# Kernel optimization log

Hardware: AMD Instinct MI355X
Metric: run time of the kernel (lower is better)

Reference implementation:

```python
import jax, jax.numpy as jnp
import numpy as np

BETA = 1.0
EPS = 1e-12  # F.normalize eps

def _normalize(x):
    # F.normalize(x, dim=1): x shape (B, N, 1)
    n = jnp.sqrt(jnp.sum(x * x, axis=1, keepdims=True))
    return x / jnp.maximum(n, EPS)

def _step(M, x):
    return _normalize(jnp.matmul(M, x))

def _eigval(M, x):
    # x^T M x / ||x||^2, x: (B, N, 1)
    Mx = jnp.matmul(M, x)                          # (B, N, 1)
    num = jnp.sum(Mx * x, axis=(1, 2))             # (B,)
    den = jnp.sum(x * x, axis=(1, 2))              # (B,)
    return num / den

def setup_inputs() -> dict:
    key = jax.random.key(0)
    kA, kx = jax.random.split(key)
    A = jax.random.normal(kA, (64, 512, 28, 28), dtype=jnp.float32)
    x0 = jax.random.normal(kx, (64, 512, 1), dtype=jnp.float32)
    return {"A": A, "x0": x0}

def reference(A, x0):
    B, C, H, W = A.shape
    Wm = A.reshape(B, C, H * W)                    # (B, C, HW)
    AAT = jnp.einsum('bcd,bed->bce', Wm, Wm)       # (B, C, C)

    # --- dominant_eigenvalue(AAT): first call initializes last_x (no grad, 3 iters) ---
    xi = _normalize(x0)
    for _ in range(3):
        xi = _step(AAT, xi)
    xi = jax.lax.stop_gradient(xi)                 # last_x after no-grad init
    x1 = _step(AAT, xi)                            # 1 differentiable iter
    largest = _eigval(AAT, x1)                     # (B,)
    last_x = jax.lax.stop_gradient(x1)             # self.last_x = x.detach()

    # --- dominant_eigenvalue(AAT - largest*I): reuses last_x, 1 iter ---
    I = jnp.eye(C, dtype=A.dtype)[None]            # (1, C, C)
    A2 = AAT - largest[:, None, None] * I
    x2 = _step(A2, last_x)
    tmp = _eigval(A2, x2)

    smallest = tmp + largest
    penalty = BETA * (largest / smallest - 1.0) ** 2
    return jnp.sum(penalty) / B
```

## Files before the change

### kernel.cpp

```cpp
#include <hip/hip_runtime.h>
#include <math.h>


#define BB 64
#define CC 512
#define DD 784
#define DCH 16
#define NCH 49
#define NSPLIT 8
#define F4PR 196
#define FEPS 1e-12f

__device__ __forceinline__ void gload16(const float4* gp, float4* lp) {
    __builtin_amdgcn_global_load_lds(
        (const __attribute__((address_space(1))) void*)gp,
        (__attribute__((address_space(3))) void*)lp, 16, 0, 0);
}

__device__ __forceinline__ float blk_reduce(float s, float* red) {
    for (int off = 32; off; off >>= 1) s += __shfl_down(s, off, 64);
    int w = threadIdx.x >> 6;
    if ((threadIdx.x & 63) == 0) red[w] = s;
    __syncthreads();
    float t = red[0] + red[1] + red[2] + red[3];
    __syncthreads();
    return t;
}

__global__ __launch_bounds__(256, 2)
void k_step(const float* __restrict__ A, const float* __restrict__ xin,
            const int nparts, float* __restrict__ vout) {
    __shared__ float xs[CC];
    __shared__ float tile[2][CC * DCH];
    __shared__ float uw[4][DCH];
    __shared__ float usd[DCH];
    __shared__ float red[4];

    const int tid = threadIdx.x;
    const int b = blockIdx.y;
    const int s = blockIdx.x;
    const int lane = tid & 63;
    const int w = tid >> 6;
    const int rr = tid >> 2, widx = tid & 3;

    const float4* Ap = (const float4*)(A + (size_t)b * CC * DD);

    {
        float4* lbase = &((float4*)tile[0])[w * 64];
        const float4* gbase = Ap + (size_t)rr * F4PR + s * 4 + widx;
#pragma unroll
        for (int i = 0; i < 8; i++)
            gload16(gbase + (size_t)i * 64 * F4PR, lbase + i * 256);
    }

    const float* xp = xin + (size_t)b * nparts * CC;
    float xv0 = 0.f, xv1 = 0.f;
    for (int p = 0; p < nparts; p++) {
        xv0 += xp[p * CC + tid];
        xv1 += xp[p * CC + tid + 256];
    }
    float ss = blk_reduce(xv0 * xv0 + xv1 * xv1, red);
    float rn = 1.0f / fmaxf(sqrtf(ss), FEPS);
    xs[tid] = xv0 * rn;
    xs[tid + 256] = xv1 * rn;

    float v0 = 0.f, v1 = 0.f;
    int buf = 0;
    const int c0 = tid, c1 = tid + 256;
    const int lh = lane >> 1;

    for (int ch = s; ch < NCH; ch += NSPLIT) {
        const int nxt = ch + NSPLIT;
        if (nxt < NCH) {
            float4* lbase = &((float4*)tile[buf ^ 1])[w * 64];
            const float4* gbase = Ap + (size_t)rr * F4PR + nxt * 4 + widx;
#pragma unroll
            for (int i = 0; i < 8; i++)
                gload16(gbase + (size_t)i * 64 * F4PR, lbase + i * 256);
            __builtin_amdgcn_sched_barrier(0);
            asm volatile("s_waitcnt vmcnt(8)" ::: "memory");
        } else {
            __builtin_amdgcn_sched_barrier(0);
            asm volatile("s_waitcnt vmcnt(0)" ::: "memory");
        }
        asm volatile("s_waitcnt lgkmcnt(0)" ::: "memory");
        __builtin_amdgcn_s_barrier();
        __builtin_amdgcn_sched_barrier(0);

        float4 ua = make_float4(0.f, 0.f, 0.f, 0.f);
        const float4* t4p = (const float4*)tile[buf];
#pragma unroll
        for (int i = 0; i < 8; i++) {
            float4 a4 = t4p[tid + i * 256];
            float x = xs[rr + i * 64];
            ua.x += a4.x * x; ua.y += a4.y * x;
            ua.z += a4.z * x; ua.w += a4.w * x;
        }
#pragma unroll
        for (int off = 4; off <= 32; off <<= 1) {
            ua.x += __shfl_xor(ua.x, off, 64);
            ua.y += __shfl_xor(ua.y, off, 64);
            ua.z += __shfl_xor(ua.z, off, 64);
            ua.w += __shfl_xor(ua.w, off, 64);
        }
        if (lane < 4) {
            uw[w][lane * 4 + 0] = ua.x; uw[w][lane * 4 + 1] = ua.y;
            uw[w][lane * 4 + 2] = ua.z; uw[w][lane * 4 + 3] = ua.w;
        }
        __builtin_amdgcn_sched_barrier(0);
        asm volatile("s_waitcnt lgkmcnt(0)" ::: "memory");
        __builtin_amdgcn_s_barrier();
        __builtin_amdgcn_sched_barrier(0);

        if (tid < DCH)
            usd[tid] = uw[0][tid] + uw[1][tid] + uw[2][tid] + uw[3][tid];
        __builtin_amdgcn_sched_barrier(0);
        asm volatile("s_waitcnt lgkmcnt(0)" ::: "memory");
        __builtin_amdgcn_s_barrier();
        __builtin_amdgcn_sched_barrier(0);

        const float* tp = tile[buf];
#pragma unroll
        for (int k = 0; k < DCH; k++) {
            int d = (k + lh) & (DCH - 1);
            float ud = usd[d];
            v0 += tp[c0 * DCH + d] * ud;
            v1 += tp[c1 * DCH + d] * ud;
        }
        __builtin_amdgcn_sched_barrier(0);
        asm volatile("s_waitcnt lgkmcnt(0)" ::: "memory");
        __builtin_amdgcn_s_barrier();
        __builtin_amdgcn_sched_barrier(0);
        buf ^= 1;
    }

    float* vp = vout + ((size_t)b * NSPLIT + s) * CC;
    vp[c0] = v0;
    vp[c1] = v1;
}

__global__ void k_mid(const float* __restrict__ t4, const float* __restrict__ t5,
                      float* __restrict__ acc, float* __restrict__ y) {
    __shared__ float red[4];
    int b = blockIdx.x;
    const float* p4 = t4 + (size_t)b * NSPLIT * CC;
    const float* p5 = t5 + (size_t)b * NSPLIT * CC;
    float a0 = 0.f, a1 = 0.f, b0 = 0.f, b1 = 0.f;
    for (int p = 0; p < NSPLIT; p++) {
        a0 += p4[p * CC + threadIdx.x]; a1 += p4[p * CC + threadIdx.x + 256];
        b0 += p5[p * CC + threadIdx.x]; b1 += p5[p * CC + threadIdx.x + 256];
    }
    float ss4 = blk_reduce(a0 * a0 + a1 * a1, red);
    float rn = 1.0f / fmaxf(sqrtf(ss4), FEPS);
    float x10 = a0 * rn, x11 = a1 * rn;
    float num = blk_reduce(b0 * x10 + b1 * x11, red);
    float den = blk_reduce(x10 * x10 + x11 * x11, red);
    float largest = num / den;
    float* yp = y + (size_t)b * CC;
    yp[threadIdx.x] = b0 - largest * x10;
    yp[threadIdx.x + 256] = b1 - largest * x11;
    if (threadIdx.x == 0) acc[b * 8 + 0] = largest;
}

__global__ void k_fin2(const float* __restrict__ w, const float* __restrict__ y,
                       float* __restrict__ acc) {
    __shared__ float red[4];
    int b = blockIdx.x;
    const float* wp = w + (size_t)b * NSPLIT * CC;
    const float* yp = y + (size_t)b * CC;
    float w0 = 0.f, w1 = 0.f;
    for (int p = 0; p < NSPLIT; p++) {
        w0 += wp[p * CC + threadIdx.x];
        w1 += wp[p * CC + threadIdx.x + 256];
    }
    float y0 = yp[threadIdx.x], y1 = yp[threadIdx.x + 256];
    float ssy = blk_reduce(y0 * y0 + y1 * y1, red);
    float rn = 1.0f / fmaxf(sqrtf(ssy), FEPS);
    float x20 = y0 * rn, x21 = y1 * rn;
    float dotwx = blk_reduce(w0 * x20 + w1 * x21, red);
    float den2 = blk_reduce(x20 * x20 + x21 * x21, red);
    if (threadIdx.x == 0) { acc[b * 8 + 1] = dotwx; acc[b * 8 + 2] = den2; }
}

__global__ void k_out(const float* __restrict__ acc, float* __restrict__ out) {
    int b = threadIdx.x;
    float largest = acc[b * 8 + 0];
    float dotwx   = acc[b * 8 + 1];
    float den2    = acc[b * 8 + 2];
    float tmp = (dotwx - largest * den2) / den2;
    float smallest = tmp + largest;
    float r = largest / smallest - 1.0f;
    float pen = r * r;
    for (int off = 32; off; off >>= 1) pen += __shfl_down(pen, off, 64);
    if (b == 0) out[0] = pen / (float)BB;
}

extern "C" void kernel_launch(void* const* d_in, const int* in_sizes, int n_in,
                              void* d_out, int out_size, void* d_ws, size_t ws_size,
                              hipStream_t stream) {
    const float* A  = (const float*)d_in[0];
    const float* x0 = (const float*)d_in[1];
    float* out = (float*)d_out;
    float* ws = (float*)d_ws;

    float* acc = ws;
    float* y   = ws + 512;
    float* PA  = y + BB * CC;
    float* PB  = PA + BB * NSPLIT * CC;

    dim3 gS(NSPLIT, BB);
    k_step<<<gS, 256, 0, stream>>>(A, x0, 1, PA);
    k_step<<<gS, 256, 0, stream>>>(A, PA, NSPLIT, PB);
    k_step<<<gS, 256, 0, stream>>>(A, PB, NSPLIT, PA);
    k_step<<<gS, 256, 0, stream>>>(A, PA, NSPLIT, PB);
    k_step<<<gS, 256, 0, stream>>>(A, PB, NSPLIT, PA);

    k_mid<<<BB, 256, 0, stream>>>(PB, PA, acc, y);

    k_step<<<gS, 256, 0, stream>>>(A, y, 1, PB);

    k_fin2<<<BB, 256, 0, stream>>>(PB, y, acc);
    k_out<<<1, 64, 0, stream>>>(acc, out);
}
```

Measured before the change: 324.8 us.

## Repack A into chunk-contiguous layout and vectorize second GEMV LDS reads

Adds a repack kernel that rewrites A per batch into contiguous 512x16 column chunks, so each step kernel streams fully contiguous memory instead of strided row segments. The step kernels switch to 7 splits of 7 contiguous chunks each and read the tile as float4 in the second reduction, with a per-wave copy of the u vector that removes one block barrier. The cost is an extra full pass over A (read and write of about 100MB) per call and a large workspace, with a fallback to the old layout when the workspace is too small.

```diff
diff --git a/kernel.cpp b/kernel.cpp
--- a/kernel.cpp
+++ b/kernel.cpp
@@ -6,9 +6,11 @@
 #define CC 512
 #define DD 784
 #define DCH 16
-#define NCH 49
-#define NSPLIT 8
+#define NSPLIT 7
+#define NCHPS 7
 #define F4PR 196
+#define CHF4 2048
+#define BF4 100352
 #define FEPS 1e-12f
 
 __device__ __forceinline__ void gload16(const float4* gp, float4* lp) {
@@ -27,31 +29,64 @@
     return t;
 }
 
+__global__ __launch_bounds__(256, 3)
+void k_repack(const float* __restrict__ A, float* __restrict__ T) {
+    __shared__ float4 st4[4 * 784];
+    const int tid = threadIdx.x, lane = tid & 63, w = tid >> 6;
+    const int b = blockIdx.y, slab = blockIdx.x;
+    const int R = slab * 16 + w * 4;
+    const float4* src = (const float4*)A + ((size_t)b * CC + R) * F4PR;
+    float4* stw = st4 + w * 784;
+#pragma unroll
+    for (int i = 0; i < 12; i++)
+        gload16(src + i * 64 + lane, stw + i * 64);
+    if (lane < 16) gload16(src + 768 + lane, stw + 768);
+    __builtin_amdgcn_sched_barrier(0);
+    asm volatile("s_waitcnt vmcnt(0)" ::: "memory");
+    __builtin_amdgcn_sched_barrier(0);
+    float4* dst = (float4*)T + (size_t)b * BF4;
+#pragma unroll
+    for (int i = 0; i < 13; i++) {
+        int m = i * 64 + lane;
+        if (m < 784) {
+            int ch = m >> 4, rem = m & 15, r = rem >> 2, dq = rem & 3;
+            dst[(size_t)ch * CHF4 + (size_t)(R + r) * 4 + dq] =
+                stw[r * 196 + ch * 4 + dq];
+        }
+    }
+}
+
+template <bool RP>
 __global__ __launch_bounds__(256, 2)
-void k_step(const float* __restrict__ A, const float* __restrict__ xin,
+void k_step(const float* __restrict__ M, const float* __restrict__ xin,
             const int nparts, float* __restrict__ vout) {
-    __shared__ float xs[CC];
-    __shared__ float tile[2][CC * DCH];
-    __shared__ float uw[4][DCH];
-    __shared__ float usd[DCH];
-    __shared__ float red[4];
+    __shared__ float4 tile4[2][CHF4];
+    __shared__ float  xs[CC];
+    __shared__ float  uw[4][16];
+    __shared__ float4 usdw4[4][4];
+    __shared__ float  red[4];
 
     const int tid = threadIdx.x;
-    const int b = blockIdx.y;
-    const int s = blockIdx.x;
-    const int lane = tid & 63;
-    const int w = tid >> 6;
+    const int b = blockIdx.y, s = blockIdx.x;
+    const int lane = tid & 63, w = tid >> 6;
     const int rr = tid >> 2, widx = tid & 3;
-
-    const float4* Ap = (const float4*)(A + (size_t)b * CC * DD);
-
-    {
-        float4* lbase = &((float4*)tile[0])[w * 64];
-        const float4* gbase = Ap + (size_t)rr * F4PR + s * 4 + widx;
-#pragma unroll
-        for (int i = 0; i < 8; i++)
-            gload16(gbase + (size_t)i * 64 * F4PR, lbase + i * 256);
-    }
+    const float4* Mb = (const float4*)M + (size_t)b * BF4;
+
+    auto issue = [&](int ch, int bufi) {
+        float4* lb = &tile4[bufi][w * 64];
+        if (RP) {
+            const float4* g = Mb + (size_t)ch * CHF4 + tid;
+#pragma unroll
+            for (int i = 0; i < 8; i++) gload16(g + i * 256, lb + i * 256);
+        } else {
+            const float4* g = Mb + (size_t)rr * F4PR + ch * 4 + widx;
+#pragma unroll
+            for (int i = 0; i < 8; i++)
+                gload16(g + (size_t)i * 64 * F4PR, lb + i * 256);
+        }
+    };
+
+    issue(s * NCHPS, 0);
 
     const float* xp = xin + (size_t)b * nparts * CC;
     float xv0 = 0.f, xv1 = 0.f;
@@ -65,18 +100,13 @@
     xs[tid + 256] = xv1 * rn;
 
     float v0 = 0.f, v1 = 0.f;
-    int buf = 0;
     const int c0 = tid, c1 = tid + 256;
-    const int lh = lane >> 1;
-
-    for (int ch = s; ch < NCH; ch += NSPLIT) {
-        const int nxt = ch + NSPLIT;
-        if (nxt < NCH) {
-            float4* lbase = &((float4*)tile[buf ^ 1])[w * 64];
-            const float4* gbase = Ap + (size_t)rr * F4PR + nxt * 4 + widx;
-#pragma unroll
-            for (int i = 0; i < 8; i++)
-                gload16(gbase + (size_t)i * 64 * F4PR, lbase + i * 256);
+    const int stag = (lane >> 1) & 3;
+
+    for (int j = 0; j < NCHPS; j++) {
+        const int buf = j & 1;
+        if (j < NCHPS - 1) {
+            issue(s * NCHPS + j + 1, buf ^ 1);
             __builtin_amdgcn_sched_barrier(0);
             asm volatile("s_waitcnt vmcnt(8)" ::: "memory");
         } else {
@@ -88,10 +118,10 @@
         __builtin_amdgcn_sched_barrier(0);
 
         float4 ua = make_float4(0.f, 0.f, 0.f, 0.f);
-        const float4* t4p = (const float4*)tile[buf];
+        const float4* tp = tile4[buf];
 #pragma unroll
         for (int i = 0; i < 8; i++) {
-            float4 a4 = t4p[tid + i * 256];
+            float4 a4 = tp[tid + i * 256];
             float x = xs[rr + i * 64];
             ua.x += a4.x * x; ua.y += a4.y * x;
             ua.z += a4.z * x; ua.w += a4.w * x;
@@ -112,26 +142,26 @@
         __builtin_amdgcn_s_barrier();
         __builtin_amdgcn_sched_barrier(0);
 
-        if (tid < DCH)
-            usd[tid] = uw[0][tid] + uw[1][tid] + uw[2][tid] + uw[3][tid];
+        if (lane < 16)
+            ((float*)usdw4[w])[lane] =
+                uw[0][lane] + uw[1][lane] + uw[2][lane] + uw[3][lane];
+        asm volatile("s_waitcnt lgkmcnt(0)" ::: "memory");
+        __builtin_amdgcn_sched_barrier(0);
+
+        const float4* up = usdw4[w];
+#pragma unroll
+        for (int qq = 0; qq < 4; qq++) {
+            int q = (qq + stag) & 3;
+            float4 u = up[q];
+            float4 a = tp[c0 * 4 + q];
+            float4 bq = tp[c1 * 4 + q];
+            v0 += a.x * u.x + a.y * u.y + a.z * u.z + a.w * u.w;
+            v1 += bq.x * u.x + bq.y * u.y + bq.z * u.z + bq.w * u.w;
+        }
         __builtin_amdgcn_sched_barrier(0);
         asm volatile("s_waitcnt lgkmcnt(0)" ::: "memory");
         __builtin_amdgcn_s_barrier();
         __builtin_amdgcn_sched_barrier(0);
-
-        const float* tp = tile[buf];
-#pragma unroll
-        for (int k = 0; k < DCH; k++) {
-            int d = (k + lh) & (DCH - 1);
-            float ud = usd[d];
-            v0 += tp[c0 * DCH + d] * ud;
-            v1 += tp[c1 * DCH + d] * ud;
-        }
-        __builtin_amdgcn_sched_barrier(0);
-        asm volatile("s_waitcnt lgkmcnt(0)" ::: "memory");
-        __builtin_amdgcn_s_barrier();
-        __builtin_amdgcn_sched_barrier(0);
-        buf ^= 1;
     }
 
     float* vp = vout + ((size_t)b * NSPLIT + s) * CC;
@@ -207,18 +237,29 @@
     float* y   = ws + 512;
     float* PA  = y + BB * CC;
     float* PB  = PA + BB * NSPLIT * CC;
+    float* T   = PB + BB * NSPLIT * CC;
+    const size_t need = ((size_t)492032 + (size_t)BB * BF4 * 4) * sizeof(float);
 
     dim3 gS(NSPLIT, BB);
-    k_step<<<gS, 256, 0, stream>>>(A, x0, 1, PA);
-    k_step<<<gS, 256, 0, stream>>>(A, PA, NSPLIT, PB);
-    k_step<<<gS, 256, 0, stream>>>(A, PB, NSPLIT, PA);
-    k_step<<<gS, 256, 0, stream>>>(A, PA, NSPLIT, PB);
-    k_step<<<gS, 256, 0, stream>>>(A, PB, NSPLIT, PA);
-
-    k_mid<<<BB, 256, 0, stream>>>(PB, PA, acc, y);
-
-    k_step<<<gS, 256, 0, stream>>>(A, y, 1, PB);
-
-    k_fin2<<<BB, 256, 0, stream>>>(PB, y, acc);
+    if (ws_size >= need) {
+        k_repack<<<dim3(32, BB), 256, 0, stream>>>(A, T);
+        k_step<true><<<gS, 256, 0, stream>>>(T, x0, 1, PA);
+        k_step<true><<<gS, 256, 0, stream>>>(T, PA, NSPLIT, PB);
+        k_step<true><<<gS, 256, 0, stream>>>(T, PB, NSPLIT, PA);
+        k_step<true><<<gS, 256, 0, stream>>>(T, PA, NSPLIT, PB);
+        k_step<true><<<gS, 256, 0, stream>>>(T, PB, NSPLIT, PA);
+        k_mid<<<BB, 256, 0, stream>>>(PB, PA, acc, y);
+        k_step<true><<<gS, 256, 0, stream>>>(T, y, 1, PB);
+        k_fin2<<<BB, 256, 0, stream>>>(PB, y, acc);
+    } else {
+        k_step<false><<<gS, 256, 0, stream>>>(A, x0, 1, PA);
+        k_step<false><<<gS, 256, 0, stream>>>(A, PA, NSPLIT, PB);
+        k_step<false><<<gS, 256, 0, stream>>>(A, PB, NSPLIT, PA);
+        k_step<false><<<gS, 256, 0, stream>>>(A, PA, NSPLIT, PB);
+        k_step<false><<<gS, 256, 0, stream>>>(A, PB, NSPLIT, PA);
+        k_mid<<<BB, 256, 0, stream>>>(PB, PA, acc, y);
+        k_step<false><<<gS, 256, 0, stream>>>(A, y, 1, PB);
+        k_fin2<<<BB, 256, 0, stream>>>(PB, y, acc);
+    }
     k_out<<<1, 64, 0, stream>>>(acc, out);
 }
```

Result: slower. 371.4 us (+14.3%).
